# Optimization experiments

Hardware: AMD Instinct MI355X
Metric: run time of the kernel (lower is better)

The kernel has to match this reference:

```python
import jax, jax.numpy as jnp
import numpy as np

B, N, C = 512, 200, 512
NH, WS = 8, 5  # num_heads, window size (window_size=(5,1), W=1 so w-axis is trivial)
HD = C // NH
SCALE = HD ** -0.5


def setup_inputs() -> dict:
    key = jax.random.key(0)
    k0, k1, k2 = jax.random.split(key, 3)
    std = C ** -0.5
    return {
        "x": jax.random.normal(k0, (B, N, C), dtype=jnp.float32),
        "qkv_w": jax.random.normal(k1, (C, 3 * C), dtype=jnp.float32) * std,
        "qkv_b": jnp.zeros((3 * C,), dtype=jnp.float32),
        "proj_w": jax.random.normal(k2, (C, C), dtype=jnp.float32) * std,
        "proj_b": jnp.zeros((C,), dtype=jnp.float32),
    }


def reference(x, qkv_w, qkv_b, proj_w, proj_b):
    b, n, c = x.shape
    g = n // WS  # number of windows along the 200-token axis (w_group == 1)
    # window partition: since W=1 and window_size[1]=1, partition is a pure reshape
    xw = x.reshape(b * g, WS, c)
    qkv = xw @ qkv_w + qkv_b                      # [b*g, WS, 3C]
    qkv = qkv.reshape(b * g, WS, 3, NH, HD)
    q, k, v = jnp.moveaxis(qkv, 2, 0)             # each [b*g, WS, NH, HD]
    q = jnp.swapaxes(q, 1, 2)                     # [b*g, NH, WS, HD]
    k = jnp.swapaxes(k, 1, 2)
    v = jnp.swapaxes(v, 1, 2)
    attn = jnp.einsum("gnqd,gnkd->gnqk", q, k) * SCALE
    attn = jax.nn.softmax(attn, axis=-1)
    o = jnp.einsum("gnqk,gnkd->gnqd", attn, v)    # [b*g, NH, WS, HD]
    o = jnp.swapaxes(o, 1, 2).reshape(b, n, c)    # window reverse (pure reshape)
    return o @ proj_w + proj_b
```

## Files before the change

### kernel.cpp

```cpp
#include <hip/hip_runtime.h>
#include <stdint.h>


typedef unsigned short u16;
typedef __bf16 bf16_t;
typedef bf16_t bf16x8 __attribute__((ext_vector_type(8)));
typedef float f32x4 __attribute__((ext_vector_type(4)));
typedef u16 u16x8 __attribute__((ext_vector_type(8)));

__device__ __forceinline__ float b2f(u16 u) {
  return __uint_as_float(((uint32_t)u) << 16);
}
__device__ __forceinline__ u16 f2b(float f) {
  uint32_t u = __float_as_uint(f);
  u += 0x7FFFu + ((u >> 16) & 1u);
  return (u16)(u >> 16);
}

#define GLOAD_LDS16(g, l)                                     \
  __builtin_amdgcn_global_load_lds(                           \
      (const __attribute__((address_space(1))) void*)(g),     \
      (__attribute__((address_space(3))) void*)(l), 16, 0, 0)

__global__ void k_sniff_bias(const uint32_t* __restrict__ x,
                             const void* __restrict__ qb,
                             const void* __restrict__ pb,
                             uint32_t* __restrict__ flag,
                             u16* __restrict__ bq, u16* __restrict__ bp) {
  __shared__ uint32_t fsh;
  if (threadIdx.x == 0) {
    int cnt = 0;
    for (int i = 0; i < 256; ++i) {
      uint32_t e = (x[i] >> 23) & 0xFFu;
      if (e >= 64u && e <= 192u) ++cnt;
    }
    uint32_t fl = (cnt >= 128) ? 1u : 0u;
    *flag = fl;
    fsh = fl;
  }
  __syncthreads();
  const bool f = fsh != 0;
  for (int i = threadIdx.x; i < 2048; i += 1024) {
    if (i < 1536)
      bq[i] = f ? f2b(((const float*)qb)[i]) : ((const u16*)qb)[i];
    else {
      int j = i - 1536;
      bp[j] = f ? f2b(((const float*)pb)[j]) : ((const u16*)pb)[j];
    }
  }
}

__global__ void k_prep_w2(const void* __restrict__ qkvw,
                          const void* __restrict__ projw,
                          u16* __restrict__ wq, u16* __restrict__ wp,
                          const uint32_t* __restrict__ flag) {
  __shared__ u16 tile[32][33];
  const bool f = (*flag) != 0;
  int bxi = blockIdx.x;
  const void* in;
  u16* out;
  int Cc;
  if (bxi < 48) {
    in = qkvw; out = wq; Cc = 1536;
  } else {
    bxi -= 48; in = projw; out = wp; Cc = 512;
  }
  const int R = 512;
  const int bx = bxi * 32, by = blockIdx.y * 32;
  const int tx = threadIdx.x, ty = threadIdx.y;
  for (int i = ty; i < 32; i += 8) {
    size_t idx = (size_t)(by + i) * Cc + bx + tx;
    tile[i][tx] = f ? f2b(((const float*)in)[idx]) : ((const u16*)in)[idx];
  }
  __syncthreads();
  for (int i = ty; i < 32; i += 8)
    out[(size_t)(bx + i) * R + by + tx] = tile[tx][i];
}

__global__ void k_conv_x(const float* __restrict__ x, u16* __restrict__ xb,
                         const uint32_t* __restrict__ flag, int n) {
  if ((*flag) == 0) return;
  int i = (blockIdx.x * 256 + threadIdx.x) * 8;
  if (i >= n) return;
  float4 a = *(const float4*)&x[i];
  float4 b = *(const float4*)&x[i + 4];
  u16x8 o;
  o[0] = f2b(a.x); o[1] = f2b(a.y); o[2] = f2b(a.z); o[3] = f2b(a.w);
  o[4] = f2b(b.x); o[5] = f2b(b.y); o[6] = f2b(b.z); o[7] = f2b(b.w);
  *(u16x8*)&xb[i] = o;
}

#define BM 256
#define BN 256
#define BK 32

__global__ __launch_bounds__(512, 2) void gemm_bt_bias(
    const u16* __restrict__ A0,
    const u16* __restrict__ A1,
    const u16* __restrict__ Bt, const u16* __restrict__ bias,
    void* __restrict__ Cout, const uint32_t* __restrict__ flag,
    int N, int K, int out_f32_if_flag) {
  __shared__ u16 smem[32768];

  const bool f = (*flag) != 0;
  const u16* A = f ? A1 : A0;

  const int t = threadIdx.x;
  const int wave = t >> 6;
  const int lane = t & 63;
  const int waveM = wave >> 2;
  const int waveN = wave & 3;

  const int nbx = gridDim.x;
  const int nwg = nbx * gridDim.y;
  const int bid = blockIdx.y * nbx + blockIdx.x;
  const int cpx = nwg >> 3;
  const int swz = (bid & 7) * cpx + (bid >> 3);
  const int bm = (swz / nbx) * BM;
  const int bn = (swz % nbx) * BN;

  const int kq = (lane >> 4) * 8;
  const int l15 = lane & 15;

  const int srow = lane >> 2;
  const int scol = (lane & 3) * 8;
  const int j0 = wave * 2;

  const u16* Agp = &A[(size_t)(bm + j0 * 16 + srow) * K + scol];
  const u16* Bgp = &Bt[(size_t)(bn + j0 * 16 + srow) * K + scol];

#define STAGE(b, k0)                                              \
  {                                                               \
    u16* as_ = smem + (b) * 16384 + j0 * 512;                     \
    u16* bs_ = smem + (b) * 16384 + 8192 + j0 * 512;              \
    GLOAD_LDS16(Agp + (size_t)(k0), as_);                         \
    GLOAD_LDS16(Agp + (size_t)(k0) + 16 * (size_t)K, as_ + 512);  \
    GLOAD_LDS16(Bgp + (size_t)(k0), bs_);                         \
    GLOAD_LDS16(Bgp + (size_t)(k0) + 16 * (size_t)K, bs_ + 512);  \
  }

  f32x4 acc[8][4] = {};

#define COMPUTE(b)                                                        \
  {                                                                       \
    const u16* As_ = smem + (b) * 16384;                                  \
    const u16* Bs_ = As_ + 8192;                                          \
    bf16x8 af[8], bfr[4];                                                 \
    _Pragma("unroll") for (int i = 0; i < 8; ++i)                         \
        af[i] = *(const bf16x8*)&As_[(waveM * 128 + i * 16 + l15) * BK + kq]; \
    _Pragma("unroll") for (int j = 0; j < 4; ++j)                         \
        bfr[j] = *(const bf16x8*)&Bs_[(waveN * 64 + j * 16 + l15) * BK + kq]; \
    _Pragma("unroll") for (int i = 0; i < 8; ++i)                         \
        _Pragma("unroll") for (int j = 0; j < 4; ++j)                     \
            acc[i][j] = __builtin_amdgcn_mfma_f32_16x16x32_bf16(          \
                af[i], bfr[j], acc[i][j], 0, 0, 0);                       \
  }

  const int NSTEP = K / BK;
  STAGE(0, 0);
  __syncthreads();
  for (int s = 0; s + 2 < NSTEP; s += 2) {
    STAGE(1, (s + 1) * BK);
    COMPUTE(0);
    __syncthreads();
    STAGE(0, (s + 2) * BK);
    COMPUTE(1);
    __syncthreads();
  }
  STAGE(1, (NSTEP - 1) * BK);
  COMPUTE(0);
  __syncthreads();
  COMPUTE(1);
  __syncthreads();

  float biasf[4];
#pragma unroll
  for (int j = 0; j < 4; ++j)
    biasf[j] = b2f(bias[bn + waveN * 64 + j * 16 + l15]);

  if (out_f32_if_flag && f) {
    float* C = (float*)Cout;
#pragma unroll
    for (int i = 0; i < 8; ++i) {
      const int row0 = waveM * 128 + i * 16 + (lane >> 4) * 4;
#pragma unroll
      for (int j = 0; j < 4; ++j) {
        const int col = waveN * 64 + j * 16 + l15;
#pragma unroll
        for (int r = 0; r < 4; ++r)
          C[(size_t)(bm + row0 + r) * N + bn + col] = acc[i][j][r] + biasf[j];
      }
    }
  } else {
    u16* C = (u16*)Cout;
#pragma unroll
    for (int h = 0; h < 2; ++h) {
      if (waveM == h) {
#pragma unroll
        for (int i = 0; i < 8; ++i) {
          const int row0 = i * 16 + (lane >> 4) * 4;
#pragma unroll
          for (int j = 0; j < 4; ++j) {
            const int col = waveN * 64 + j * 16 + l15;
#pragma unroll
            for (int r = 0; r < 4; ++r)
              smem[(row0 + r) * 256 + col] = f2b(acc[i][j][r] + biasf[j]);
          }
        }
      }
      __syncthreads();
#pragma unroll
      for (int s = 0; s < 8; ++s) {
        const int vi = s * 512 + t;
        const int row = vi >> 5;
        const int col = (vi & 31) * 8;
        u16x8 v = *(const u16x8*)&smem[row * 256 + col];
        *(u16x8*)&C[(size_t)(bm + h * 128 + row) * N + bn + col] = v;
      }
      __syncthreads();
    }
  }
#undef STAGE
#undef COMPUTE
}

__global__ __launch_bounds__(256) void attn_win(const u16* __restrict__ qkv,
                                                u16* __restrict__ o,
                                                int nwin) {
  const int w = blockIdx.x * 4 + (threadIdx.x >> 6);
  if (w >= nwin) return;
  const int lane = threadIdx.x & 63;
  const int h = lane >> 3;
  const int d0 = (lane & 7) * 8;
  const u16* base = qkv + (size_t)w * (5 * 1536) + h * 64 + d0;

  float qf[5][8], kf[5][8], vf[5][8];
#pragma unroll
  for (int i = 0; i < 5; ++i) {
    u16x8 vq = *(const u16x8*)&base[i * 1536];
    u16x8 vk = *(const u16x8*)&base[i * 1536 + 512];
    u16x8 vv = *(const u16x8*)&base[i * 1536 + 1024];
#pragma unroll
    for (int e = 0; e < 8; ++e) {
      qf[i][e] = b2f(vq[e]);
      kf[i][e] = b2f(vk[e]);
      vf[i][e] = b2f(vv[e]);
    }
  }

  float s[5][5];
#pragma unroll
  for (int i = 0; i < 5; ++i)
#pragma unroll
    for (int j = 0; j < 5; ++j) {
      float acc = 0.f;
#pragma unroll
      for (int e = 0; e < 8; ++e) acc += qf[i][e] * kf[j][e];
      s[i][j] = acc;
    }
#pragma unroll
  for (int off = 1; off < 8; off <<= 1) {
#pragma unroll
    for (int i = 0; i < 5; ++i)
#pragma unroll
      for (int j = 0; j < 5; ++j) s[i][j] += __shfl_xor(s[i][j], off, 64);
  }

  const float SCALE = 0.125f;
  u16* ob = o + (size_t)w * (5 * 512) + h * 64 + d0;
#pragma unroll
  for (int i = 0; i < 5; ++i) {
    float m = s[i][0];
#pragma unroll
    for (int j = 1; j < 5; ++j) m = fmaxf(m, s[i][j]);
    float e0[5], l = 0.f;
#pragma unroll
    for (int j = 0; j < 5; ++j) {
      e0[j] = __expf((s[i][j] - m) * SCALE);
      l += e0[j];
    }
    const float rl = 1.f / l;
    u16x8 out;
#pragma unroll
    for (int e = 0; e < 8; ++e) {
      float acc = 0.f;
#pragma unroll
      for (int j = 0; j < 5; ++j) acc += e0[j] * vf[j][e];
      out[e] = f2b(acc * rl);
    }
    *(u16x8*)&ob[i * 512] = out;
  }
}

extern "C" void kernel_launch(void* const* d_in, const int* in_sizes, int n_in,
                              void* d_out, int out_size, void* d_ws,
                              size_t ws_size, hipStream_t stream) {
  const void* x      = d_in[0];
  const void* qkv_w  = d_in[1];
  const void* qkv_b  = d_in[2];
  const void* proj_w = d_in[3];
  const void* proj_b = d_in[4];

  const int M = 102400, K = 512, N1 = 1536, N2 = 512;

  const size_t fixed = 8192 + 1572864 + 524288 + (size_t)M * 512 * 2;
  int CH = 4;
  if (ws_size >= fixed + (size_t)M * 2048 * 2) CH = 1;
  else if (ws_size >= fixed + (size_t)(M / 2) * 2048 * 2) CH = 2;
  const int MC = M / CH;

  char* ws = (char*)d_ws;
  uint32_t* flag = (uint32_t*)ws;
  u16* bq      = (u16*)(ws + 256);
  u16* bp      = (u16*)(ws + 256 + 3072);
  u16* wt_qkv  = (u16*)(ws + 8192);
  u16* wt_proj = (u16*)(ws + 8192 + 1572864);
  u16* attnb   = (u16*)(ws + 8192 + 1572864 + 524288);
  u16* qkvc    = (u16*)((char*)attnb + (size_t)M * 512 * 2);
  u16* xbc     = (u16*)((char*)qkvc + (size_t)MC * 1536 * 2);

  k_sniff_bias<<<1, 1024, 0, stream>>>((const uint32_t*)x, qkv_b, proj_b, flag,
                                       bq, bp);
  k_prep_w2<<<dim3(64, 16), dim3(32, 8), 0, stream>>>(qkv_w, proj_w, wt_qkv,
                                                      wt_proj, flag);
  for (int c = 0; c < CH; ++c) {
    const size_t roff = (size_t)c * MC * 512;
    k_conv_x<<<MC * 512 / 2048, 256, 0, stream>>>((const float*)x + roff, xbc,
                                                  flag, MC * 512);
    gemm_bt_bias<<<dim3(N1 / BN, MC / BM), 512, 0, stream>>>(
        (const u16*)x + roff, xbc, wt_qkv, bq, qkvc, flag, N1, K, 0);
    attn_win<<<(MC / 5) / 4, 256, 0, stream>>>(qkvc, (u16*)attnb + roff,
                                               MC / 5);
  }
  gemm_bt_bias<<<dim3(N2 / BN, M / BM), 512, 0, stream>>>(
      attnb, attnb, wt_proj, bp, d_out, flag, N2, K, 1);
}
```

Baseline: 778.0 us.

## Restructure GEMM mainloop into 4-phase pipelined schedule with BK=64 and priority hints

Result: no change. 768.7 us (-1.2%).

```diff
diff --git a/kernel.cpp b/kernel.cpp
--- a/kernel.cpp
+++ b/kernel.cpp
@@ -92,15 +92,14 @@
 
 #define BM 256
 #define BN 256
-#define BK 32
-
-__global__ __launch_bounds__(512, 2) void gemm_bt_bias(
+
+__global__ __launch_bounds__(512, 1) void gemm_bt_bias(
     const u16* __restrict__ A0,
     const u16* __restrict__ A1,
     const u16* __restrict__ Bt, const u16* __restrict__ bias,
     void* __restrict__ Cout, const uint32_t* __restrict__ flag,
     int N, int K, int out_f32_if_flag) {
-  __shared__ u16 smem[32768];
+  __shared__ u16 smem[65536];
 
   const bool f = (*flag) != 0;
   const u16* A = f ? A1 : A0;
@@ -119,58 +118,79 @@
   const int bm = (swz / nbx) * BM;
   const int bn = (swz % nbx) * BN;
 
-  const int kq = (lane >> 4) * 8;
   const int l15 = lane & 15;
-
-  const int srow = lane >> 2;
-  const int scol = (lane & 3) * 8;
-  const int j0 = wave * 2;
-
-  const u16* Agp = &A[(size_t)(bm + j0 * 16 + srow) * K + scol];
-  const u16* Bgp = &Bt[(size_t)(bn + j0 * 16 + srow) * K + scol];
-
-#define STAGE(b, k0)                                              \
-  {                                                               \
-    u16* as_ = smem + (b) * 16384 + j0 * 512;                     \
-    u16* bs_ = smem + (b) * 16384 + 8192 + j0 * 512;              \
-    GLOAD_LDS16(Agp + (size_t)(k0), as_);                         \
-    GLOAD_LDS16(Agp + (size_t)(k0) + 16 * (size_t)K, as_ + 512);  \
-    GLOAD_LDS16(Bgp + (size_t)(k0), bs_);                         \
-    GLOAD_LDS16(Bgp + (size_t)(k0) + 16 * (size_t)K, bs_ + 512);  \
+  const int rdOff = ((lane >> 5) & 1) * 256 + l15 * 16 + ((lane >> 4) & 1) * 8;
+  const int rowS = (lane >> 1) & 15;
+  const int colS = ((lane >> 5) & 1) * 16 + (lane & 1) * 8;
+  const u16* AgS[4];
+  const u16* BgS[4];
+#pragma unroll
+  for (int q = 0; q < 4; ++q) {
+    const int c = wave * 4 + q, g = c >> 1, p = c & 1;
+    AgS[q] = &A[(size_t)(bm + g * 16 + rowS) * K + p * 32 + colS];
+    BgS[q] = &Bt[(size_t)(bn + g * 16 + rowS) * K + p * 32 + colS];
   }
 
   f32x4 acc[8][4] = {};
-
-#define COMPUTE(b)                                                        \
-  {                                                                       \
-    const u16* As_ = smem + (b) * 16384;                                  \
-    const u16* Bs_ = As_ + 8192;                                          \
-    bf16x8 af[8], bfr[4];                                                 \
-    _Pragma("unroll") for (int i = 0; i < 8; ++i)                         \
-        af[i] = *(const bf16x8*)&As_[(waveM * 128 + i * 16 + l15) * BK + kq]; \
-    _Pragma("unroll") for (int j = 0; j < 4; ++j)                         \
-        bfr[j] = *(const bf16x8*)&Bs_[(waveN * 64 + j * 16 + l15) * BK + kq]; \
-    _Pragma("unroll") for (int i = 0; i < 8; ++i)                         \
-        _Pragma("unroll") for (int j = 0; j < 4; ++j)                     \
-            acc[i][j] = __builtin_amdgcn_mfma_f32_16x16x32_bf16(          \
-                af[i], bfr[j], acc[i][j], 0, 0, 0);                       \
-  }
-
-  const int NSTEP = K / BK;
-  STAGE(0, 0);
-  __syncthreads();
-  for (int s = 0; s + 2 < NSTEP; s += 2) {
-    STAGE(1, (s + 1) * BK);
-    COMPUTE(0);
-    __syncthreads();
-    STAGE(0, (s + 2) * BK);
-    COMPUTE(1);
-    __syncthreads();
-  }
-  STAGE(1, (NSTEP - 1) * BK);
-  COMPUTE(0);
-  __syncthreads();
-  COMPUTE(1);
+  const int NT = K / 64;
+
+#define STAGE_OP(PTRS, dstU16, kN)                                          \
+  {                                                                         \
+    _Pragma("unroll") for (int q = 0; q < 4; ++q)                           \
+        GLOAD_LDS16(PTRS[q] + (kN), &smem[(dstU16) + (wave * 4 + q) * 512]); \
+  }
+
+#define PHASE(MH, NH, STAGECODE, TAILWAIT)                                   \
+  {                                                                          \
+    bf16x8 af[4][2], bfr[2][2];                                              \
+    _Pragma("unroll") for (int ii = 0; ii < 4; ++ii)                         \
+        _Pragma("unroll") for (int ks = 0; ks < 2; ++ks)                     \
+            af[ii][ks] = *(const bf16x8*)&smem[ab +                          \
+                (waveM * 8 + (MH) * 4 + ii) * 1024 + ks * 512 + rdOff];      \
+    _Pragma("unroll") for (int jj = 0; jj < 2; ++jj)                         \
+        _Pragma("unroll") for (int ks = 0; ks < 2; ++ks)                     \
+            bfr[jj][ks] = *(const bf16x8*)&smem[bb +                         \
+                (waveN * 4 + (NH) * 2 + jj) * 1024 + ks * 512 + rdOff];      \
+    STAGECODE;                                                               \
+    asm volatile("" ::: "memory");                                           \
+    __builtin_amdgcn_s_barrier();                                            \
+    asm volatile("" ::: "memory");                                           \
+    __builtin_amdgcn_s_setprio(1);                                           \
+    _Pragma("unroll") for (int ii = 0; ii < 4; ++ii)                         \
+        _Pragma("unroll") for (int jj = 0; jj < 2; ++jj)                     \
+            _Pragma("unroll") for (int ks = 0; ks < 2; ++ks)                 \
+                acc[(MH) * 4 + ii][(NH) * 2 + jj] =                          \
+                    __builtin_amdgcn_mfma_f32_16x16x32_bf16(                 \
+                        af[ii][ks], bfr[jj][ks],                             \
+                        acc[(MH) * 4 + ii][(NH) * 2 + jj], 0, 0, 0);         \
+    __builtin_amdgcn_s_setprio(0);                                           \
+    TAILWAIT;                                                                \
+    asm volatile("" ::: "memory");                                           \
+    __builtin_amdgcn_s_barrier();                                            \
+    asm volatile("" ::: "memory");                                           \
+  }
+
+  STAGE_OP(AgS, 0, 0);
+  STAGE_OP(BgS, 16384, 0);
+  asm volatile("s_waitcnt vmcnt(0)" ::: "memory");
+  __builtin_amdgcn_s_barrier();
+  asm volatile("" ::: "memory");
+
+  for (int tt = 0; tt < NT; ++tt) {
+    const int ab = (tt & 1) * 32768;
+    const int bb = ab + 16384;
+    const int sab = ((tt + 1) & 1) * 32768;
+    const int sbb = sab + 16384;
+    const int kN = (tt + 1) * 64;
+    const bool st = (tt + 1) < NT;
+    PHASE(0, 0, if (st) STAGE_OP(AgS, sab, kN), )
+    PHASE(0, 1, if (st) STAGE_OP(BgS, sbb, kN), )
+    PHASE(1, 0, , )
+    PHASE(1, 1, , asm volatile("s_waitcnt vmcnt(0)" ::: "memory"))
+  }
+#undef PHASE
+#undef STAGE_OP
+
   __syncthreads();
 
   float biasf[4];
@@ -220,8 +240,6 @@
       __syncthreads();
     }
   }
-#undef STAGE
-#undef COMPUTE
 }
 
 __global__ __launch_bounds__(256) void attn_win(const u16* __restrict__ qkv,
```
